# Kernel optimization log

Measured on AMD Instinct MI355X. Metric: run time of the kernel, lower is better.

Reference implementation:

```python
import jax, jax.numpy as jnp
import numpy as np

N_VOX = 200_000
C = 64
B, G = 2, 128  # batch size, grid resolution per axis
K = 27         # 3x3x3 kernel volume
EPS = 1e-5


def _build_coords_and_kernel_map(seed=0):
    """Build unique voxel coords on a [B,G,G,G] grid and the 27-offset kernel map.

    nbr[i, k] = row index of the voxel at coord[i] + offset[k], or N_VOX if absent
    (sentinel row that gathers zeros). This mirrors MinkowskiEngine's
    coordinate-hash in/out kernel maps for a stride-1 conv.
    """
    rng = np.random.default_rng(seed)
    total = B * G * G * G
    keys = np.sort(rng.choice(total, size=N_VOX, replace=False).astype(np.int64))
    z = keys % G
    y = (keys // G) % G
    x = (keys // (G * G)) % G
    b = keys // (G * G * G)
    offs = [(dx, dy, dz) for dx in (-1, 0, 1) for dy in (-1, 0, 1) for dz in (-1, 0, 1)]
    nbr = np.full((N_VOX, K), N_VOX, dtype=np.int64)
    for k, (dx, dy, dz) in enumerate(offs):
        nx, ny, nz = x + dx, y + dy, z + dz
        valid = (nx >= 0) & (nx < G) & (ny >= 0) & (ny < G) & (nz >= 0) & (nz < G)
        nkey = ((b * G + nx) * G + ny) * G + nz
        pos = np.clip(np.searchsorted(keys, nkey), 0, N_VOX - 1)
        found = valid & (keys[pos] == nkey)
        nbr[:, k] = np.where(found, pos, N_VOX)
    return jnp.asarray(nbr)


def setup_inputs() -> dict:
    key = jax.random.key(0)
    ks = jax.random.split(key, 12)
    w_scale = 1.0 / np.sqrt(K * C)
    inp = {
        "feats": jax.random.normal(ks[0], (N_VOX, C), jnp.float32),
        "nbr": _build_coords_and_kernel_map(),
        "W1": jax.random.normal(ks[1], (K, C, C), jnp.float32) * w_scale,
        "g1": 1.0 + 0.1 * jax.random.normal(ks[2], (C,), jnp.float32),
        "b1": 0.1 * jax.random.normal(ks[3], (C,), jnp.float32),
        "m1": 0.1 * jax.random.normal(ks[4], (C,), jnp.float32),
        "v1": jax.random.uniform(ks[5], (C,), jnp.float32, 0.5, 1.5),
        "W2": jax.random.normal(ks[6], (K, C, C), jnp.float32) * w_scale,
        "g2": 1.0 + 0.1 * jax.random.normal(ks[7], (C,), jnp.float32),
        "b2": 0.1 * jax.random.normal(ks[8], (C,), jnp.float32),
        "m2": 0.1 * jax.random.normal(ks[9], (C,), jnp.float32),
        "v2": jax.random.uniform(ks[10], (C,), jnp.float32, 0.5, 1.5),
    }
    return inp


def _bn(x, g, b, m, v):
    # MinkowskiBatchNorm, eval mode: per-channel affine with running stats
    return (x - m) * (g * jax.lax.rsqrt(v + EPS)) + b


def _sparse_conv(feats, nbr, W):
    # gather-GEMM-scatter sparse 3D conv over the precomputed kernel map.
    # Sentinel index N_VOX gathers the appended zero row (missing neighbor).
    fpad = jnp.concatenate([feats, jnp.zeros((1, feats.shape[1]), feats.dtype)], axis=0)
    out = jnp.zeros((feats.shape[0], W.shape[2]), feats.dtype)
    for k in range(W.shape[0]):  # fixed 27-tap loop (structural, not data dim)
        out = out + fpad[nbr[:, k]] @ W[k]
    return out


def reference(feats, nbr, W1, g1, b1, m1, v1, W2, g2, b2, m2, v2):
    h = jax.nn.relu(_bn(_sparse_conv(feats, nbr, W1), g1, b1, m1, v1))
    h = _bn(_sparse_conv(h, nbr, W2), g2, b2, m2, v2)
    # in_channels == out_channels and stride == 1 -> identity shortcut
    return jax.nn.relu(h + feats)
```

## Files before the change

kernel.cpp:

```cpp
#include <hip/hip_runtime.h>
#include <hip/hip_bf16.h>

#define NVOX 200000
#define NTAP 27
#define OSTR 68
#define ROWB 128

typedef __bf16          bf16x8 __attribute__((ext_vector_type(8)));
typedef unsigned short  u16x8  __attribute__((ext_vector_type(8)));
typedef float           f32x4  __attribute__((ext_vector_type(4)));

#define FB_BYTES    ((size_t)(NVOX + 1) * ROWB)
#define WSHUF_BYTES (NTAP * 2 * 4 * 64 * 16)
#define FB_OFF      0
#define H_OFF       (FB_BYTES)
#define WS1_OFF     (2 * FB_BYTES)
#define WS2_OFF     (WS1_OFF + WSHUF_BYTES)
#define FLAG_OFF    (WS2_OFF + WSHUF_BYTES)

static __device__ __forceinline__ unsigned short f2bf_bits(float f) {
    __hip_bfloat16 h = __float2bfloat16(f);
    union { __hip_bfloat16 h; unsigned short u; } u; u.h = h; return u.u;
}
static __device__ __forceinline__ float bf2f(unsigned short s) {
    union { float f; unsigned u; } u; u.u = ((unsigned)s) << 16; return u.f;
}
static __device__ __forceinline__ float ld_param(const void* p, int c, int isbf) {
    return isbf ? bf2f(((const unsigned short*)p)[c]) : ((const float*)p)[c];
}
static __device__ __forceinline__ void gload_lds16(const void* gp, void* lp) {
    __builtin_amdgcn_global_load_lds(
        (const __attribute__((address_space(1))) void*)gp,
        (__attribute__((address_space(3))) void*)lp, 16, 0, 0);
}
static __device__ __forceinline__ int wave_isbf(const unsigned* v1w) {
    int l = threadIdx.x & 63;
    int ok = 1;
    if (l < 32) {
        unsigned w = v1w[l], lo = w & 0xFFFFu, hi = w >> 16;
        ok = (lo >= 0x3F00u && lo <= 0x3FC0u && hi >= 0x3F00u && hi <= 0x3FC0u);
    }
    return __all(ok);
}

__global__ __launch_bounds__(256)
void prep_kernel(const void* __restrict__ feats,
                 const void* __restrict__ W1, const void* __restrict__ W2,
                 const unsigned* __restrict__ v1w, const unsigned* __restrict__ nbrw,
                 uint4* __restrict__ fbuf, uint4* __restrict__ hbuf,
                 uint4* __restrict__ Ws1, uint4* __restrict__ Ws2,
                 int* __restrict__ flags) {
    const int bx = blockIdx.x;
    if (bx < 6250) {
        const int isbf = wave_isbf(v1w);
        size_t t = (size_t)bx * 256 + threadIdx.x;
        if (isbf) {
            fbuf[t] = ((const uint4*)feats)[t];
        } else {
            float4 a = ((const float4*)feats)[2 * t];
            float4 b = ((const float4*)feats)[2 * t + 1];
            union { uint4 q; unsigned short u[8]; } o;
            o.u[0] = f2bf_bits(a.x); o.u[1] = f2bf_bits(a.y);
            o.u[2] = f2bf_bits(a.z); o.u[3] = f2bf_bits(a.w);
            o.u[4] = f2bf_bits(b.x); o.u[5] = f2bf_bits(b.y);
            o.u[6] = f2bf_bits(b.z); o.u[7] = f2bf_bits(b.w);
            fbuf[t] = o.q;
        }
    } else if (bx < 6358) {
        const int isbf = wave_isbf(v1w);
        int t = (bx - 6250) * 256 + threadIdx.x;
        const void* W = (t < 13824) ? W1 : W2;
        uint4* Ws     = (t < 13824) ? Ws1 : Ws2;
        int f = (t < 13824) ? t : t - 13824;
        int k  = f / 512;
        int r  = f % 512;
        int kc = r / 256;
        int r2 = r % 256;
        int nc = r2 / 64;
        int l  = r2 % 64;
        int quad = l >> 4, li = l & 15;
        unsigned short tmp[8];
#pragma unroll
        for (int j = 0; j < 8; ++j) {
            int off = k * 4096 + (kc * 32 + quad * 8 + j) * 64 + (nc * 16 + li);
            tmp[j] = isbf ? ((const unsigned short*)W)[off]
                          : f2bf_bits(((const float*)W)[off]);
        }
        uint4 v;
        v.x = (unsigned)tmp[0] | ((unsigned)tmp[1] << 16);
        v.y = (unsigned)tmp[2] | ((unsigned)tmp[3] << 16);
        v.z = (unsigned)tmp[4] | ((unsigned)tmp[5] << 16);
        v.w = (unsigned)tmp[6] | ((unsigned)tmp[7] << 16);
        Ws[f] = v;
    } else {
        int t = threadIdx.x;
        if (t < 64) {
            int isbf = wave_isbf(v1w);
            int n64ok = 1;
#pragma unroll
            for (int i = 0; i < 8; ++i)
                if (nbrw[2 * (t * 8 + i) + 1] != 0u) n64ok = 0;
            int n64 = __all(n64ok);
            if (t == 0) { flags[0] = isbf; flags[1] = n64; }
        }
        uint4 z = make_uint4(0u, 0u, 0u, 0u);
        if (t >= 64 && t < 72) fbuf[(size_t)NVOX * 8 + (t - 64)] = z;
        if (t >= 72 && t < 80) hbuf[(size_t)NVOX * 8 + (t - 72)] = z;
    }
}

#define STG(kk, bp) do {                                                    \
    if ((mgw >> (kk)) & 1) {                                                \
        int ia_ = nbrLDS[r0 * NTAP + (kk)];                                 \
        int ib_ = nbrLDS[r1 * NTAP + (kk)];                                 \
        gload_lds16(srcB + (size_t)ia_ * ROWB + f0 * 16,                    \
                    (void*)((bp) + w * 128));                               \
        gload_lds16(srcB + (size_t)ib_ * ROWB + f1 * 16,                    \
                    (void*)((bp) + w * 128 + 64));                         \
    } } while (0)

#define LOADB(kk, B0r, B1r) do {                                            \
    B0r = Ws[(kk) * 512 + w * 64 + l];                                      \
    B1r = Ws[(kk) * 512 + 256 + w * 64 + l];                                \
} while (0)

#define COMPUTE(kk, bp, B0, B1) do {                                        \
    _Pragma("unroll")                                                       \
    for (int g = 0; g < 4; ++g) {                                           \
        if ((mg[g] >> (kk)) & 1) {                                          \
            bf16x8 a0_ = *(const bf16x8*)((bp) + ro0[g]);                   \
            bf16x8 a1_ = *(const bf16x8*)((bp) + ro1[g]);                   \
            acc[g] = __builtin_amdgcn_mfma_f32_16x16x32_bf16(a0_, B0, acc[g], 0, 0, 0); \
            acc[g] = __builtin_amdgcn_mfma_f32_16x16x32_bf16(a1_, B1, acc[g], 0, 0, 0); \
        }                                                                   \
    }                                                                       \
} while (0)

#define SEP asm volatile("" ::: "memory")
#define WB2 asm volatile("s_waitcnt vmcnt(2)\n\ts_barrier" ::: "memory")

__global__ __launch_bounds__(256, 7)
void conv_bn_kernel(const uint4* __restrict__ srcV,
                    const void* __restrict__ nbr,
                    const bf16x8* __restrict__ Ws,
                    const void* __restrict__ gg, const void* __restrict__ bb,
                    const void* __restrict__ mm, const void* __restrict__ vv,
                    const u16x8* __restrict__ resid,
                    const int* __restrict__ flags,
                    void* __restrict__ dst, int final_out) {
    __shared__ __align__(16) int smi[5828];
    int*   nbrLDS = smi;
    uint4* at0    = (uint4*)(smi + 1728);
    uint4* at1    = at0 + 512;
    int*   maskLDS = smi + 5824;
    float* outLDS = (float*)smi;

    const int tid  = threadIdx.x;
    const int nwg  = gridDim.x;
    const int orig = blockIdx.x;
    const int qq   = nwg >> 3, rr = nwg & 7;
    const int xcd  = orig & 7, idx = orig >> 3;
    const int bid  = (xcd < rr ? xcd * (qq + 1) : rr * (qq + 1) + (xcd - rr) * qq) + idx;
    const int base = bid * 64;

    const int isbf = flags[0];
    const int n64  = flags[1];
    const char* srcB = (const char*)srcV;

    if (tid < 4) maskLDS[tid] = 0;
    __syncthreads();
    {
        if (!n64) {
            const int* np = (const int*)nbr + (long)base * NTAP;
            for (int i = tid; i < 64 * NTAP; i += 256) nbrLDS[i] = np[i];
        } else {
            const long long* np = (const long long*)nbr + (long)base * NTAP;
            for (int i = tid; i < 64 * NTAP; i += 256) nbrLDS[i] = (int)np[i];
        }
    }
    __syncthreads();

    if (tid < NTAP * 4) {
        int k = tid >> 2, g = tid & 3;
        int mn = 0x7fffffff;
#pragma unroll
        for (int r = 0; r < 16; ++r) mn = min(mn, nbrLDS[(g * 16 + r) * NTAP + k]);
        if (mn < NVOX) atomicOr(&maskLDS[g], 1 << k);
    }
    __syncthreads();

    const int w = tid >> 6, l = tid & 63;
    const int quad = l >> 4, li = l & 15;

    int mg[4];
#pragma unroll
    for (int g = 0; g < 4; ++g) mg[g] = __builtin_amdgcn_readfirstlane(maskLDS[g]);
    const int mgw = __builtin_amdgcn_readfirstlane(maskLDS[w]);

    const int s0 = w * 128 + l;
    const int s1 = s0 + 64;
    const int r0 = s0 >> 3, f0 = (s0 - r0) & 7;
    const int r1 = s1 >> 3, f1 = (s1 - r1) & 7;
    int ro0[4], ro1[4];
#pragma unroll
    for (int g = 0; g < 4; ++g) {
        int row = g * 16 + li;
        ro0[g] = row * 8 + ((quad + row) & 7);
        ro1[g] = row * 8 + ((quad + 4 + row) & 7);
    }

    f32x4 acc[4];
#pragma unroll
    for (int g = 0; g < 4; ++g) acc[g] = (f32x4){0.f, 0.f, 0.f, 0.f};

    bf16x8 xB0, xB1, yB0, yB1;

    STG(0, at0); SEP;
    LOADB(0, xB0, xB1);

    for (int k = 0; k < 26; k += 2) {
        WB2;
        STG(k + 1, at1); SEP;
        LOADB(k + 1, yB0, yB1);
        COMPUTE(k, at0, xB0, xB1);
        WB2;
        STG(k + 2, at0); SEP;
        LOADB(k + 2, xB0, xB1);
        COMPUTE(k + 1, at1, yB0, yB1);
    }
    WB2;
    COMPUTE(26, at0, xB0, xB1);

    const int c = w * 16 + li;
    float scale = ld_param(gg, c, isbf) * rsqrtf(ld_param(vv, c, isbf) + 1e-5f);
    float offs  = ld_param(bb, c, isbf) - ld_param(mm, c, isbf) * scale;

    __syncthreads();
#pragma unroll
    for (int g = 0; g < 4; ++g)
#pragma unroll
        for (int r = 0; r < 4; ++r)
            outLDS[(g * 16 + quad * 4 + r) * OSTR + c] = acc[g][r] * scale + offs;
    __syncthreads();

    {
        int trow = tid >> 2, cc = tid & 3;
        long grow = base + trow;
        const float4* lp = (const float4*)&outLDS[trow * OSTR + cc * 16];
        float4 q0 = lp[0], q1 = lp[1], q2 = lp[2], q3 = lp[3];
        float vals[16] = {q0.x, q0.y, q0.z, q0.w, q1.x, q1.y, q1.z, q1.w,
                          q2.x, q2.y, q2.z, q2.w, q3.x, q3.y, q3.z, q3.w};

        if (resid) {
            const u16x8* rp = resid + grow * 8 + cc * 2;
            u16x8 r0v = rp[0], r1v = rp[1];
#pragma unroll
            for (int j = 0; j < 8; ++j) { vals[j] += bf2f(r0v[j]); vals[8 + j] += bf2f(r1v[j]); }
        }
#pragma unroll
        for (int j = 0; j < 16; ++j) vals[j] = fmaxf(vals[j], 0.f);

        const int store_bf = (!final_out) || isbf;
        if (store_bf) {
            u16x8 o0, o1;
#pragma unroll
            for (int j = 0; j < 8; ++j) { o0[j] = f2bf_bits(vals[j]); o1[j] = f2bf_bits(vals[8 + j]); }
            u16x8* dp = (u16x8*)dst + grow * 8 + cc * 2;
            dp[0] = o0; dp[1] = o1;
        } else {
            float4* dp = (float4*)dst + grow * 16 + cc * 4;
            dp[0] = (float4){vals[0], vals[1], vals[2], vals[3]};
            dp[1] = (float4){vals[4], vals[5], vals[6], vals[7]};
            dp[2] = (float4){vals[8], vals[9], vals[10], vals[11]};
            dp[3] = (float4){vals[12], vals[13], vals[14], vals[15]};
        }
    }
}

extern "C" void kernel_launch(void* const* d_in, const int* in_sizes, int n_in,
                              void* d_out, int out_size, void* d_ws, size_t ws_size,
                              hipStream_t stream) {
    const void* feats = d_in[0];
    const void* nbr   = d_in[1];
    const void* W1    = d_in[2];
    const void* g1    = d_in[3];
    const void* b1    = d_in[4];
    const void* m1    = d_in[5];
    const void* v1    = d_in[6];
    const void* W2    = d_in[7];
    const void* g2    = d_in[8];
    const void* b2    = d_in[9];
    const void* m2    = d_in[10];
    const void* v2    = d_in[11];

    char* ws = (char*)d_ws;
    uint4* fbuf = (uint4*)(ws + FB_OFF);
    uint4* hbuf = (uint4*)(ws + H_OFF);
    uint4* Ws1  = (uint4*)(ws + WS1_OFF);
    uint4* Ws2  = (uint4*)(ws + WS2_OFF);
    int*   flags = (int*)(ws + FLAG_OFF);

    prep_kernel<<<dim3(6359), dim3(256), 0, stream>>>(
        feats, W1, W2, (const unsigned*)v1, (const unsigned*)nbr,
        fbuf, hbuf, Ws1, Ws2, flags);

    conv_bn_kernel<<<dim3(NVOX / 64), dim3(256), 0, stream>>>(
        fbuf, nbr, (const bf16x8*)Ws1, g1, b1, m1, v1,
        nullptr, flags, hbuf, 0);

    conv_bn_kernel<<<dim3(NVOX / 64), dim3(256), 0, stream>>>(
        hbuf, nbr, (const bf16x8*)Ws2, g2, b2, m2, v2,
        (const u16x8*)fbuf, flags, d_out, 1);
}
```

Baseline: 250.1 us.

## Compact valid neighbor pairs per tap and scatter MFMA results via LDS atomics

Switches the sparse conv from dense per-row tap processing to a compacted pair list. Each 1024-thread block handles 250 voxels and buckets the valid (neighbor, output-row) pairs per tap into 16-row segments. Waves then take segments, gather A rows straight from global memory, run MFMAs against the tap's weights, and accumulate results into an LDS output tile with float atomics. This removes MFMA work and staging for missing neighbors. The cost is LDS atomic traffic, less global-to-LDS prefetch overlap, and a hard cap of 64 pairs per tap per block that silently drops contributions on denser inputs.

Result: slower. 646.9 us (+158.7%).

```diff
diff --git a/kernel.cpp b/kernel.cpp
--- a/kernel.cpp
+++ b/kernel.cpp
@@ -3,8 +3,9 @@
 
 #define NVOX 200000
 #define NTAP 27
-#define OSTR 68
 #define ROWB 128
+#define VPB  250
+#define OST  66
 
 typedef __bf16          bf16x8 __attribute__((ext_vector_type(8)));
 typedef unsigned short  u16x8  __attribute__((ext_vector_type(8)));
@@ -27,11 +28,6 @@
 }
 static __device__ __forceinline__ float ld_param(const void* p, int c, int isbf) {
     return isbf ? bf2f(((const unsigned short*)p)[c]) : ((const float*)p)[c];
-}
-static __device__ __forceinline__ void gload_lds16(const void* gp, void* lp) {
-    __builtin_amdgcn_global_load_lds(
-        (const __attribute__((address_space(1))) void*)gp,
-        (__attribute__((address_space(3))) void*)lp, 16, 0, 0);
 }
 static __device__ __forceinline__ int wave_isbf(const unsigned* v1w) {
     int l = threadIdx.x & 63;
@@ -109,37 +105,7 @@
     }
 }
 
-#define STG(kk, bp) do {                                                    \
-    if ((mgw >> (kk)) & 1) {                                                \
-        int ia_ = nbrLDS[r0 * NTAP + (kk)];                                 \
-        int ib_ = nbrLDS[r1 * NTAP + (kk)];                                 \
-        gload_lds16(srcB + (size_t)ia_ * ROWB + f0 * 16,                    \
-                    (void*)((bp) + w * 128));                               \
-        gload_lds16(srcB + (size_t)ib_ * ROWB + f1 * 16,                    \
-                    (void*)((bp) + w * 128 + 64));                         \
-    } } while (0)
-
-#define LOADB(kk, B0r, B1r) do {                                            \
-    B0r = Ws[(kk) * 512 + w * 64 + l];                                      \
-    B1r = Ws[(kk) * 512 + 256 + w * 64 + l];                                \
-} while (0)
-
-#define COMPUTE(kk, bp, B0, B1) do {                                        \
-    _Pragma("unroll")                                                       \
-    for (int g = 0; g < 4; ++g) {                                           \
-        if ((mg[g] >> (kk)) & 1) {                                          \
-            bf16x8 a0_ = *(const bf16x8*)((bp) + ro0[g]);                   \
-            bf16x8 a1_ = *(const bf16x8*)((bp) + ro1[g]);                   \
-            acc[g] = __builtin_amdgcn_mfma_f32_16x16x32_bf16(a0_, B0, acc[g], 0, 0, 0); \
-            acc[g] = __builtin_amdgcn_mfma_f32_16x16x32_bf16(a1_, B1, acc[g], 0, 0, 0); \
-        }                                                                   \
-    }                                                                       \
-} while (0)
-
-#define SEP asm volatile("" ::: "memory")
-#define WB2 asm volatile("s_waitcnt vmcnt(2)\n\ts_barrier" ::: "memory")
-
-__global__ __launch_bounds__(256, 7)
+__global__ __launch_bounds__(1024, 4)
 void conv_bn_kernel(const uint4* __restrict__ srcV,
                     const void* __restrict__ nbr,
                     const bf16x8* __restrict__ Ws,
@@ -148,131 +114,155 @@
                     const u16x8* __restrict__ resid,
                     const int* __restrict__ flags,
                     void* __restrict__ dst, int final_out) {
-    __shared__ __align__(16) int smi[5828];
-    int*   nbrLDS = smi;
-    uint4* at0    = (uint4*)(smi + 1728);
-    uint4* at1    = at0 + 512;
-    int*   maskLDS = smi + 5824;
-    float* outLDS = (float*)smi;
-
-    const int tid  = threadIdx.x;
+    __shared__ __align__(16) float outLDS[VPB * OST];
+    __shared__ __align__(16) int   pool[26 * 64 + 256];
+    __shared__ int   cnt[27];
+    __shared__ int   segs[136];
+    __shared__ int   nsegA[1];
+    __shared__ float scOff[128];
+
+    const int tid = threadIdx.x;
     const int nwg  = gridDim.x;
     const int orig = blockIdx.x;
     const int qq   = nwg >> 3, rr = nwg & 7;
     const int xcd  = orig & 7, idx = orig >> 3;
     const int bid  = (xcd < rr ? xcd * (qq + 1) : rr * (qq + 1) + (xcd - rr) * qq) + idx;
-    const int base = bid * 64;
+    const int base = bid * VPB;
 
     const int isbf = flags[0];
     const int n64  = flags[1];
     const char* srcB = (const char*)srcV;
 
-    if (tid < 4) maskLDS[tid] = 0;
+    for (int i = tid; i < VPB * OST; i += 1024) outLDS[i] = 0.0f;
+    if (tid < 27) cnt[tid] = 0;
+    if (tid < 64) {
+        float sc = ld_param(gg, tid, isbf) * rsqrtf(ld_param(vv, tid, isbf) + 1e-5f);
+        scOff[tid]      = sc;
+        scOff[64 + tid] = ld_param(bb, tid, isbf) - ld_param(mm, tid, isbf) * sc;
+    }
     __syncthreads();
+
     {
-        if (!n64) {
-            const int* np = (const int*)nbr + (long)base * NTAP;
-            for (int i = tid; i < 64 * NTAP; i += 256) nbrLDS[i] = np[i];
-        } else {
-            const long long* np = (const long long*)nbr + (long)base * NTAP;
-            for (int i = tid; i < 64 * NTAP; i += 256) nbrLDS[i] = (int)np[i];
-        }
+        const int ebase = base * NTAP;
+        for (int e = tid; e < VPB * NTAP; e += 1024) {
+            int src;
+            if (!n64) src = ((const int*)nbr)[ebase + e];
+            else      src = (int)((const long long*)nbr)[ebase + e];
+            int i = e / NTAP;
+            int k = e - i * NTAP;
+            if (k != 13 && src < NVOX) {
+                int kk = k - (k > 13 ? 1 : 0);
+                int p = atomicAdd(&cnt[k], 1);
+                if (p < 64) pool[kk * 64 + p] = src * 256 + i;
+            }
+        }
+        if (tid < VPB)           pool[26 * 64 + tid] = (base + tid) * 256 + tid;
+        else if (tid < 256)      pool[26 * 64 + tid] = NVOX * 256;
     }
     __syncthreads();
 
-    if (tid < NTAP * 4) {
-        int k = tid >> 2, g = tid & 3;
-        int mn = 0x7fffffff;
-#pragma unroll
-        for (int r = 0; r < 16; ++r) mn = min(mn, nbrLDS[(g * 16 + r) * NTAP + k]);
-        if (mn < NVOX) atomicOr(&maskLDS[g], 1 << k);
+    if (tid < 26 * 16) {
+        int kk = tid >> 4, p = tid & 15;
+        int k  = kk + (kk >= 13 ? 1 : 0);
+        int c  = min(cnt[k], 64);
+        int id = c + p;
+        if (id < ((c + 15) & ~15)) pool[kk * 64 + id] = NVOX * 256;
+    }
+    if (tid == 0) {
+        int ns = 0;
+        for (int kk = 0; kk < 26; ++kk) {
+            int k = kk + (kk >= 13 ? 1 : 0);
+            int c = min(cnt[k], 64);
+            for (int t = 0; t < c; t += 16) segs[ns++] = (k << 16) | (kk * 64 + t);
+        }
+        for (int t = 0; t < 256; t += 16) segs[ns++] = (13 << 16) | (26 * 64 + t);
+        nsegA[0] = ns;
     }
     __syncthreads();
 
-    const int w = tid >> 6, l = tid & 63;
-    const int quad = l >> 4, li = l & 15;
-
-    int mg[4];
-#pragma unroll
-    for (int g = 0; g < 4; ++g) mg[g] = __builtin_amdgcn_readfirstlane(maskLDS[g]);
-    const int mgw = __builtin_amdgcn_readfirstlane(maskLDS[w]);
-
-    const int s0 = w * 128 + l;
-    const int s1 = s0 + 64;
-    const int r0 = s0 >> 3, f0 = (s0 - r0) & 7;
-    const int r1 = s1 >> 3, f1 = (s1 - r1) & 7;
-    int ro0[4], ro1[4];
-#pragma unroll
-    for (int g = 0; g < 4; ++g) {
-        int row = g * 16 + li;
-        ro0[g] = row * 8 + ((quad + row) & 7);
-        ro1[g] = row * 8 + ((quad + 4 + row) & 7);
-    }
-
-    f32x4 acc[4];
-#pragma unroll
-    for (int g = 0; g < 4; ++g) acc[g] = (f32x4){0.f, 0.f, 0.f, 0.f};
-
-    bf16x8 xB0, xB1, yB0, yB1;
-
-    STG(0, at0); SEP;
-    LOADB(0, xB0, xB1);
-
-    for (int k = 0; k < 26; k += 2) {
-        WB2;
-        STG(k + 1, at1); SEP;
-        LOADB(k + 1, yB0, yB1);
-        COMPUTE(k, at0, xB0, xB1);
-        WB2;
-        STG(k + 2, at0); SEP;
-        LOADB(k + 2, xB0, xB1);
-        COMPUTE(k + 1, at1, yB0, yB1);
-    }
-    WB2;
-    COMPUTE(26, at0, xB0, xB1);
-
-    const int c = w * 16 + li;
-    float scale = ld_param(gg, c, isbf) * rsqrtf(ld_param(vv, c, isbf) + 1e-5f);
-    float offs  = ld_param(bb, c, isbf) - ld_param(mm, c, isbf) * scale;
-
-    __syncthreads();
-#pragma unroll
-    for (int g = 0; g < 4; ++g)
-#pragma unroll
-        for (int r = 0; r < 4; ++r)
-            outLDS[(g * 16 + quad * 4 + r) * OSTR + c] = acc[g][r] * scale + offs;
+    {
+        const int wid = tid >> 6, l = tid & 63;
+        const int quad = l >> 4, li = l & 15;
+        const int nseg = nsegA[0];
+        const uint4* WsU = (const uint4*)Ws;
+
+        for (int s = wid; s < nseg; s += 16) {
+            int desc = segs[s];
+            int k  = __builtin_amdgcn_readfirstlane(desc >> 16);
+            int st = __builtin_amdgcn_readfirstlane(desc & 0xFFFF);
+            int pairA = pool[st + li];
+            int srcA  = pairA >> 8;
+            const bf16x8* ap = (const bf16x8*)(srcB + (size_t)srcA * ROWB);
+            bf16x8 a0 = ap[quad];
+            bf16x8 a1 = ap[4 + quad];
+            const uint4* Bp = WsU + k * 512;
+            bf16x8 b00 = *(const bf16x8*)&Bp[      0 * 64 + l];
+            bf16x8 b01 = *(const bf16x8*)&Bp[256 + 0 * 64 + l];
+            bf16x8 b10 = *(const bf16x8*)&Bp[      1 * 64 + l];
+            bf16x8 b11 = *(const bf16x8*)&Bp[256 + 1 * 64 + l];
+            bf16x8 b20 = *(const bf16x8*)&Bp[      2 * 64 + l];
+            bf16x8 b21 = *(const bf16x8*)&Bp[256 + 2 * 64 + l];
+            bf16x8 b30 = *(const bf16x8*)&Bp[      3 * 64 + l];
+            bf16x8 b31 = *(const bf16x8*)&Bp[256 + 3 * 64 + l];
+            int4 p4 = *(const int4*)&pool[st + quad * 4];
+            f32x4 c0 = {0.f,0.f,0.f,0.f}, c1 = c0, c2 = c0, c3 = c0;
+            c0 = __builtin_amdgcn_mfma_f32_16x16x32_bf16(a0, b00, c0, 0, 0, 0);
+            c0 = __builtin_amdgcn_mfma_f32_16x16x32_bf16(a1, b01, c0, 0, 0, 0);
+            c1 = __builtin_amdgcn_mfma_f32_16x16x32_bf16(a0, b10, c1, 0, 0, 0);
+            c1 = __builtin_amdgcn_mfma_f32_16x16x32_bf16(a1, b11, c1, 0, 0, 0);
+            c2 = __builtin_amdgcn_mfma_f32_16x16x32_bf16(a0, b20, c2, 0, 0, 0);
+            c2 = __builtin_amdgcn_mfma_f32_16x16x32_bf16(a1, b21, c2, 0, 0, 0);
+            c3 = __builtin_amdgcn_mfma_f32_16x16x32_bf16(a0, b30, c3, 0, 0, 0);
+            c3 = __builtin_amdgcn_mfma_f32_16x16x32_bf16(a1, b31, c3, 0, 0, 0);
+            int r0 = (p4.x & 255) * OST + li;
+            int r1 = (p4.y & 255) * OST + li;
+            int r2 = (p4.z & 255) * OST + li;
+            int r3 = (p4.w & 255) * OST + li;
+            atomicAdd(&outLDS[r0 +  0], c0[0]); atomicAdd(&outLDS[r1 +  0], c0[1]);
+            atomicAdd(&outLDS[r2 +  0], c0[2]); atomicAdd(&outLDS[r3 +  0], c0[3]);
+            atomicAdd(&outLDS[r0 + 16], c1[0]); atomicAdd(&outLDS[r1 + 16], c1[1]);
+            atomicAdd(&outLDS[r2 + 16], c1[2]); atomicAdd(&outLDS[r3 + 16], c1[3]);
+            atomicAdd(&outLDS[r0 + 32], c2[0]); atomicAdd(&outLDS[r1 + 32], c2[1]);
+            atomicAdd(&outLDS[r2 + 32], c2[2]); atomicAdd(&outLDS[r3 + 32], c2[3]);
+            atomicAdd(&outLDS[r0 + 48], c3[0]); atomicAdd(&outLDS[r1 + 48], c3[1]);
+            atomicAdd(&outLDS[r2 + 48], c3[2]); atomicAdd(&outLDS[r3 + 48], c3[3]);
+        }
+    }
     __syncthreads();
 
     {
         int trow = tid >> 2, cc = tid & 3;
-        long grow = base + trow;
-        const float4* lp = (const float4*)&outLDS[trow * OSTR + cc * 16];
-        float4 q0 = lp[0], q1 = lp[1], q2 = lp[2], q3 = lp[3];
-        float vals[16] = {q0.x, q0.y, q0.z, q0.w, q1.x, q1.y, q1.z, q1.w,
-                          q2.x, q2.y, q2.z, q2.w, q3.x, q3.y, q3.z, q3.w};
-
-        if (resid) {
-            const u16x8* rp = resid + grow * 8 + cc * 2;
-            u16x8 r0v = rp[0], r1v = rp[1];
-#pragma unroll
-            for (int j = 0; j < 8; ++j) { vals[j] += bf2f(r0v[j]); vals[8 + j] += bf2f(r1v[j]); }
-        }
-#pragma unroll
-        for (int j = 0; j < 16; ++j) vals[j] = fmaxf(vals[j], 0.f);
-
-        const int store_bf = (!final_out) || isbf;
-        if (store_bf) {
-            u16x8 o0, o1;
-#pragma unroll
-            for (int j = 0; j < 8; ++j) { o0[j] = f2bf_bits(vals[j]); o1[j] = f2bf_bits(vals[8 + j]); }
-            u16x8* dp = (u16x8*)dst + grow * 8 + cc * 2;
-            dp[0] = o0; dp[1] = o1;
-        } else {
-            float4* dp = (float4*)dst + grow * 16 + cc * 4;
-            dp[0] = (float4){vals[0], vals[1], vals[2], vals[3]};
-            dp[1] = (float4){vals[4], vals[5], vals[6], vals[7]};
-            dp[2] = (float4){vals[8], vals[9], vals[10], vals[11]};
-            dp[3] = (float4){vals[12], vals[13], vals[14], vals[15]};
+        if (trow < VPB) {
+            long grow = base + trow;
+            float vals[16];
+#pragma unroll
+            for (int j = 0; j < 16; ++j) {
+                int c = cc * 16 + j;
+                vals[j] = outLDS[trow * OST + c] * scOff[c] + scOff[64 + c];
+            }
+            if (resid) {
+                const u16x8* rp = resid + grow * 8 + cc * 2;
+                u16x8 r0v = rp[0], r1v = rp[1];
+#pragma unroll
+                for (int j = 0; j < 8; ++j) { vals[j] += bf2f(r0v[j]); vals[8 + j] += bf2f(r1v[j]); }
+            }
+#pragma unroll
+            for (int j = 0; j < 16; ++j) vals[j] = fmaxf(vals[j], 0.f);
+
+            const int store_bf = (!final_out) || isbf;
+            if (store_bf) {
+                u16x8 o0, o1;
+#pragma unroll
+                for (int j = 0; j < 8; ++j) { o0[j] = f2bf_bits(vals[j]); o1[j] = f2bf_bits(vals[8 + j]); }
+                u16x8* dp = (u16x8*)dst + grow * 8 + cc * 2;
+                dp[0] = o0; dp[1] = o1;
+            } else {
+                float4* dp = (float4*)dst + grow * 16 + cc * 4;
+                dp[0] = (float4){vals[0], vals[1], vals[2], vals[3]};
+                dp[1] = (float4){vals[4], vals[5], vals[6], vals[7]};
+                dp[2] = (float4){vals[8], vals[9], vals[10], vals[11]};
+                dp[3] = (float4){vals[12], vals[13], vals[14], vals[15]};
+            }
         }
     }
 }
@@ -304,11 +294,11 @@
         feats, W1, W2, (const unsigned*)v1, (const unsigned*)nbr,
         fbuf, hbuf, Ws1, Ws2, flags);
 
-    conv_bn_kernel<<<dim3(NVOX / 64), dim3(256), 0, stream>>>(
+    conv_bn_kernel<<<dim3(NVOX / VPB), dim3(1024), 0, stream>>>(
         fbuf, nbr, (const bf16x8*)Ws1, g1, b1, m1, v1,
         nullptr, flags, hbuf, 0);
 
-    conv_bn_kernel<<<dim3(NVOX / 64), dim3(256), 0, stream>>>(
+    conv_bn_kernel<<<dim3(NVOX / VPB), dim3(1024), 0, stream>>>(
         hbuf, nbr, (const bf16x8*)Ws2, g2, b2, m2, v2,
         (const u16x8*)fbuf, flags, d_out, 1);
 }
```

## Load gathered neighbor rows directly into registers instead of staging through LDS

Applied to the files above, without the earlier changes.

Drops the double-buffered global_load_lds staging of gathered feature rows and the per-tap occupancy masks. Each wave now loads its A fragments straight from global memory through the neighbor indices and issues the MFMAs without barriers. The intent is to remove the LDS round trip, the per-tap barriers and the mask setup. In exchange, every one of the four waves now gathers the same rows redundantly (4x global/L2 traffic), MFMAs run for empty taps, the explicit software pipelining is lost, and launch bounds drop to 4 waves per SIMD.

Measured after the change: 394.7 us. 57.9% more time.

```diff
diff --git a/kernel.cpp b/kernel.cpp
--- a/kernel.cpp
+++ b/kernel.cpp
@@ -27,11 +27,6 @@
 }
 static __device__ __forceinline__ float ld_param(const void* p, int c, int isbf) {
     return isbf ? bf2f(((const unsigned short*)p)[c]) : ((const float*)p)[c];
-}
-static __device__ __forceinline__ void gload_lds16(const void* gp, void* lp) {
-    __builtin_amdgcn_global_load_lds(
-        (const __attribute__((address_space(1))) void*)gp,
-        (__attribute__((address_space(3))) void*)lp, 16, 0, 0);
 }
 static __device__ __forceinline__ int wave_isbf(const unsigned* v1w) {
     int l = threadIdx.x & 63;
@@ -109,37 +104,7 @@
     }
 }
 
-#define STG(kk, bp) do {                                                    \
-    if ((mgw >> (kk)) & 1) {                                                \
-        int ia_ = nbrLDS[r0 * NTAP + (kk)];                                 \
-        int ib_ = nbrLDS[r1 * NTAP + (kk)];                                 \
-        gload_lds16(srcB + (size_t)ia_ * ROWB + f0 * 16,                    \
-                    (void*)((bp) + w * 128));                               \
-        gload_lds16(srcB + (size_t)ib_ * ROWB + f1 * 16,                    \
-                    (void*)((bp) + w * 128 + 64));                         \
-    } } while (0)
-
-#define LOADB(kk, B0r, B1r) do {                                            \
-    B0r = Ws[(kk) * 512 + w * 64 + l];                                      \
-    B1r = Ws[(kk) * 512 + 256 + w * 64 + l];                                \
-} while (0)
-
-#define COMPUTE(kk, bp, B0, B1) do {                                        \
-    _Pragma("unroll")                                                       \
-    for (int g = 0; g < 4; ++g) {                                           \
-        if ((mg[g] >> (kk)) & 1) {                                          \
-            bf16x8 a0_ = *(const bf16x8*)((bp) + ro0[g]);                   \
-            bf16x8 a1_ = *(const bf16x8*)((bp) + ro1[g]);                   \
-            acc[g] = __builtin_amdgcn_mfma_f32_16x16x32_bf16(a0_, B0, acc[g], 0, 0, 0); \
-            acc[g] = __builtin_amdgcn_mfma_f32_16x16x32_bf16(a1_, B1, acc[g], 0, 0, 0); \
-        }                                                                   \
-    }                                                                       \
-} while (0)
-
-#define SEP asm volatile("" ::: "memory")
-#define WB2 asm volatile("s_waitcnt vmcnt(2)\n\ts_barrier" ::: "memory")
-
-__global__ __launch_bounds__(256, 7)
+__global__ __launch_bounds__(256, 4)
 void conv_bn_kernel(const uint4* __restrict__ srcV,
                     const void* __restrict__ nbr,
                     const bf16x8* __restrict__ Ws,
@@ -148,11 +113,8 @@
                     const u16x8* __restrict__ resid,
                     const int* __restrict__ flags,
                     void* __restrict__ dst, int final_out) {
-    __shared__ __align__(16) int smi[5828];
+    __shared__ __align__(16) int smi[64 * OSTR];
     int*   nbrLDS = smi;
-    uint4* at0    = (uint4*)(smi + 1728);
-    uint4* at1    = at0 + 512;
-    int*   maskLDS = smi + 5824;
     float* outLDS = (float*)smi;
 
     const int tid  = threadIdx.x;
@@ -167,8 +129,6 @@
     const int n64  = flags[1];
     const char* srcB = (const char*)srcV;
 
-    if (tid < 4) maskLDS[tid] = 0;
-    __syncthreads();
     {
         if (!n64) {
             const int* np = (const int*)nbr + (long)base * NTAP;
@@ -180,56 +140,33 @@
     }
     __syncthreads();
 
-    if (tid < NTAP * 4) {
-        int k = tid >> 2, g = tid & 3;
-        int mn = 0x7fffffff;
-#pragma unroll
-        for (int r = 0; r < 16; ++r) mn = min(mn, nbrLDS[(g * 16 + r) * NTAP + k]);
-        if (mn < NVOX) atomicOr(&maskLDS[g], 1 << k);
-    }
-    __syncthreads();
-
     const int w = tid >> 6, l = tid & 63;
     const int quad = l >> 4, li = l & 15;
 
-    int mg[4];
-#pragma unroll
-    for (int g = 0; g < 4; ++g) mg[g] = __builtin_amdgcn_readfirstlane(maskLDS[g]);
-    const int mgw = __builtin_amdgcn_readfirstlane(maskLDS[w]);
-
-    const int s0 = w * 128 + l;
-    const int s1 = s0 + 64;
-    const int r0 = s0 >> 3, f0 = (s0 - r0) & 7;
-    const int r1 = s1 >> 3, f1 = (s1 - r1) & 7;
-    int ro0[4], ro1[4];
-#pragma unroll
-    for (int g = 0; g < 4; ++g) {
-        int row = g * 16 + li;
-        ro0[g] = row * 8 + ((quad + row) & 7);
-        ro1[g] = row * 8 + ((quad + 4 + row) & 7);
-    }
-
     f32x4 acc[4];
 #pragma unroll
     for (int g = 0; g < 4; ++g) acc[g] = (f32x4){0.f, 0.f, 0.f, 0.f};
 
-    bf16x8 xB0, xB1, yB0, yB1;
-
-    STG(0, at0); SEP;
-    LOADB(0, xB0, xB1);
-
-    for (int k = 0; k < 26; k += 2) {
-        WB2;
-        STG(k + 1, at1); SEP;
-        LOADB(k + 1, yB0, yB1);
-        COMPUTE(k, at0, xB0, xB1);
-        WB2;
-        STG(k + 2, at0); SEP;
-        LOADB(k + 2, xB0, xB1);
-        COMPUTE(k + 1, at1, yB0, yB1);
-    }
-    WB2;
-    COMPUTE(26, at0, xB0, xB1);
+    const uint4* WsU = (const uint4*)Ws;
+    const int bidx0 = w * 64 + l;
+    const int nb    = li * NTAP;
+
+#pragma unroll 2
+    for (int k = 0; k < NTAP; ++k) {
+        bf16x8 B0 = *(const bf16x8*)&WsU[k * 512 + bidx0];
+        bf16x8 B1 = *(const bf16x8*)&WsU[k * 512 + 256 + bidx0];
+        int src[4];
+#pragma unroll
+        for (int g = 0; g < 4; ++g) src[g] = nbrLDS[nb + g * 16 * NTAP + k];
+#pragma unroll
+        for (int g = 0; g < 4; ++g) {
+            const bf16x8* ap = (const bf16x8*)(srcB + (size_t)src[g] * ROWB);
+            bf16x8 a0 = ap[quad];
+            bf16x8 a1 = ap[4 + quad];
+            acc[g] = __builtin_amdgcn_mfma_f32_16x16x32_bf16(a0, B0, acc[g], 0, 0, 0);
+            acc[g] = __builtin_amdgcn_mfma_f32_16x16x32_bf16(a1, B1, acc[g], 0, 0, 0);
+        }
+    }
 
     const int c = w * 16 + li;
     float scale = ld_param(gg, c, isbf) * rsqrtf(ld_param(vv, c, isbf) + 1e-5f);
```

## Read neighbor indices from global per tap instead of staging in LDS

Applied to the files above, without the earlier changes.

Drops the per-block copy of the 64x27 neighbor-index table into shared memory; each tap's gather now reads its two row indices straight from global memory, scaled for int32 or int64 layout. The freed LDS shrinks the shared footprint, and the launch bound is raised from 7 to 8 blocks per CU to allow more resident blocks. The hand-written vmcnt(2)+s_barrier sequence is replaced by plain __syncthreads. The trade-off is a dependent global load in front of every feature gather, and full barriers that may drain all outstanding loads, in exchange for less up-front staging and higher occupancy.

New measurement: 241.1 us. -3.6%, faster.

```diff
diff --git a/kernel.cpp b/kernel.cpp
--- a/kernel.cpp
+++ b/kernel.cpp
@@ -111,8 +111,8 @@
 
 #define STG(kk, bp) do {                                                    \
     if ((mgw >> (kk)) & 1) {                                                \
-        int ia_ = nbrLDS[r0 * NTAP + (kk)];                                 \
-        int ib_ = nbrLDS[r1 * NTAP + (kk)];                                 \
+        int ia_ = nbrG[o0 + (kk) * tmul];                                   \
+        int ib_ = nbrG[o1 + (kk) * tmul];                                   \
         gload_lds16(srcB + (size_t)ia_ * ROWB + f0 * 16,                    \
                     (void*)((bp) + w * 128));                               \
         gload_lds16(srcB + (size_t)ib_ * ROWB + f1 * 16,                    \
@@ -136,10 +136,7 @@
     }                                                                       \
 } while (0)
 
-#define SEP asm volatile("" ::: "memory")
-#define WB2 asm volatile("s_waitcnt vmcnt(2)\n\ts_barrier" ::: "memory")
-
-__global__ __launch_bounds__(256, 7)
+__global__ __launch_bounds__(256, 8)
 void conv_bn_kernel(const uint4* __restrict__ srcV,
                     const void* __restrict__ nbr,
                     const bf16x8* __restrict__ Ws,
@@ -148,12 +145,11 @@
                     const u16x8* __restrict__ resid,
                     const int* __restrict__ flags,
                     void* __restrict__ dst, int final_out) {
-    __shared__ __align__(16) int smi[5828];
-    int*   nbrLDS = smi;
-    uint4* at0    = (uint4*)(smi + 1728);
-    uint4* at1    = at0 + 512;
-    int*   maskLDS = smi + 5824;
-    float* outLDS = (float*)smi;
+    __shared__ __align__(16) int smi[64 * OSTR];
+    int*   maskLDS = smi;
+    uint4* at0     = (uint4*)(smi + 4);
+    uint4* at1     = at0 + 512;
+    float* outLDS  = (float*)smi;
 
     const int tid  = threadIdx.x;
     const int nwg  = gridDim.x;
@@ -167,24 +163,19 @@
     const int n64  = flags[1];
     const char* srcB = (const char*)srcV;
 
+    const int* nbrG = (const int*)nbr;
+    const int  tmul = n64 ? 2 : 1;
+    const int  smul = NTAP * tmul;
+
     if (tid < 4) maskLDS[tid] = 0;
-    __syncthreads();
-    {
-        if (!n64) {
-            const int* np = (const int*)nbr + (long)base * NTAP;
-            for (int i = tid; i < 64 * NTAP; i += 256) nbrLDS[i] = np[i];
-        } else {
-            const long long* np = (const long long*)nbr + (long)base * NTAP;
-            for (int i = tid; i < 64 * NTAP; i += 256) nbrLDS[i] = (int)np[i];
-        }
-    }
     __syncthreads();
 
     if (tid < NTAP * 4) {
         int k = tid >> 2, g = tid & 3;
+        int ofs = (base + g * 16) * smul + k * tmul;
         int mn = 0x7fffffff;
 #pragma unroll
-        for (int r = 0; r < 16; ++r) mn = min(mn, nbrLDS[(g * 16 + r) * NTAP + k]);
+        for (int r = 0; r < 16; ++r) mn = min(mn, nbrG[ofs + r * smul]);
         if (mn < NVOX) atomicOr(&maskLDS[g], 1 << k);
     }
     __syncthreads();
@@ -201,6 +192,8 @@
     const int s1 = s0 + 64;
     const int r0 = s0 >> 3, f0 = (s0 - r0) & 7;
     const int r1 = s1 >> 3, f1 = (s1 - r1) & 7;
+    const int o0 = (base + r0) * smul;
+    const int o1 = (base + r1) * smul;
     int ro0[4], ro1[4];
 #pragma unroll
     for (int g = 0; g < 4; ++g) {
@@ -215,20 +208,20 @@
 
     bf16x8 xB0, xB1, yB0, yB1;
 
-    STG(0, at0); SEP;
+    STG(0, at0);
     LOADB(0, xB0, xB1);
+    __syncthreads();
 
     for (int k = 0; k < 26; k += 2) {
-        WB2;
-        STG(k + 1, at1); SEP;
+        STG(k + 1, at1);
         LOADB(k + 1, yB0, yB1);
         COMPUTE(k, at0, xB0, xB1);
-        WB2;
-        STG(k + 2, at0); SEP;
+        __syncthreads();
+        STG(k + 2, at0);
         LOADB(k + 2, xB0, xB1);
         COMPUTE(k + 1, at1, yB0, yB1);
-    }
-    WB2;
+        __syncthreads();
+    }
     COMPUTE(26, at0, xB0, xB1);
 
     const int c = w * 16 + li;
@@ -262,11 +255,11 @@
 
         const int store_bf = (!final_out) || isbf;
         if (store_bf) {
-            u16x8 o0, o1;
-#pragma unroll
-            for (int j = 0; j < 8; ++j) { o0[j] = f2bf_bits(vals[j]); o1[j] = f2bf_bits(vals[8 + j]); }
+            u16x8 o0v, o1v;
+#pragma unroll
+            for (int j = 0; j < 8; ++j) { o0v[j] = f2bf_bits(vals[j]); o1v[j] = f2bf_bits(vals[8 + j]); }
             u16x8* dp = (u16x8*)dst + grow * 8 + cc * 2;
-            dp[0] = o0; dp[1] = o1;
+            dp[0] = o0v; dp[1] = o1v;
         } else {
             float4* dp = (float4*)dst + grow * 16 + cc * 4;
             dp[0] = (float4){vals[0], vals[1], vals[2], vals[3]};
```
